# Optimization experiments

Measured on AMD Instinct MI355X. Metric: run time of the kernel, lower is better.

## Reference

```python
import jax, jax.numpy as jnp
import numpy as np

NUM_EMBEDDINGS = 1024
EMBEDDING_DIM = 256
COMMITMENT_COST = 1.0


def setup_inputs() -> dict:
    key = jax.random.key(0)
    k_in, k_emb = jax.random.split(key)
    inputs = jax.random.normal(k_in, (64, 32, 32, EMBEDDING_DIM), dtype=jnp.float32)
    embeddings = jax.random.normal(k_emb, (NUM_EMBEDDINGS, EMBEDDING_DIM), dtype=jnp.float32)
    return {"inputs": inputs, "embeddings": embeddings}


def reference(inputs, embeddings):
    # Eval-mode forward of VectorQuantizerEMA (EMA buffer update is a no-grad
    # stateful side effect, skipped here; see notes).
    input_shape = inputs.shape
    flat = inputs.reshape(-1, EMBEDDING_DIM)                       # [N, D]
    distances = (
        jnp.sum(flat ** 2, axis=1, keepdims=True)
        + jnp.sum(embeddings ** 2, axis=1)
        - 2.0 * flat @ embeddings.T
    )
    encoding_indices = jnp.argmin(distances, axis=1)               # [N]
    # one-hot @ embeddings == gather (avoid materializing [N, K] one-hot)
    quantized = embeddings[encoding_indices].reshape(input_shape)
    e_latent_loss = jnp.mean((jax.lax.stop_gradient(quantized) - inputs) ** 2)
    loss = COMMITMENT_COST * e_latent_loss
    # straight-through estimator
    quantized_st = inputs + jax.lax.stop_gradient(quantized - inputs)
    return quantized_st, loss, encoding_indices[:, None]
```

## Files before the change

### kernel.cpp

```cpp
#include <hip/hip_runtime.h>
#include <float.h>

#define NROWS 65536
#define DK 256
#define NCODES 1024
#define FLAG_CAP 8192
#define MARGIN1 0.15f
#define D_BIAS 384.0f
#define TIE_EPS 2.0e-3f

#define LOSS_OFF 16777216
#define IDX_OFF  16777217

#define CHUNK_STRIDE 1040

#define WS_FLAG1   0
#define WS_LOSSP   8
#define WS_ENORMD  520
#define WS_ENORMF  8720
#define WS_FROWS   12816
#define WS_IDX     45584
#define WS_EHI     307728
#define WS_ET      307728

typedef _Float16 f16x8 __attribute__((ext_vector_type(8)));
typedef float f32x4 __attribute__((ext_vector_type(4)));
typedef unsigned int uint32;

__device__ __forceinline__ uint32 packh2(float a, float b) {
  return (uint32)__builtin_bit_cast(unsigned short, (_Float16)a) |
         ((uint32)__builtin_bit_cast(unsigned short, (_Float16)b) << 16);
}

__global__ __launch_bounds__(256) void init_kernel(
    const float* __restrict__ E, double* __restrict__ enorm_d,
    float* __restrict__ enorm_f, uint4* __restrict__ Ehi,
    int* __restrict__ flag1, double* __restrict__ loss_part) {
  const int t = threadIdx.x;
  const int c = blockIdx.x * 8 + (t >> 5);
  const int g = t & 31;
  if (blockIdx.x == 0) {
    if (t == 0) *flag1 = 0;
    if (t < 64) loss_part[t] = 0.0;
  }
  const float4* er4 = (const float4*)(E + (size_t)c * DK);
  const float4 va = er4[g * 2];
  const float4 vb = er4[g * 2 + 1];
  double s = (double)va.x * va.x + (double)va.y * va.y + (double)va.z * va.z + (double)va.w * va.w
           + (double)vb.x * vb.x + (double)vb.y * vb.y + (double)vb.z * vb.z + (double)vb.w * vb.w;
  uint4 h;
  h.x = packh2(va.x, va.y);
  h.y = packh2(va.z, va.w);
  h.z = packh2(vb.x, vb.y);
  h.w = packh2(vb.z, vb.w);
  const int ctg = c >> 8, cga = (c >> 4) & 15, col = c & 15;
  const int kc = g >> 2, quad = g & 3;
  Ehi[((size_t)((ctg * 8 + kc) * 16 + cga)) * 64 + (size_t)(quad * 16 + col)] = h;
  #pragma unroll
  for (int m = 1; m < 32; m <<= 1) s += __shfl_xor(s, m, 64);
  if (g == 0) {
    enorm_d[c] = s;
    enorm_f[c] = (float)s;
  }
}

__global__ __launch_bounds__(256, 3) void dist_fused(
    const float* __restrict__ X, const uint4* __restrict__ Ehi,
    const float* __restrict__ E, const float* __restrict__ enorm_f,
    int* __restrict__ idx_ws, int* __restrict__ flag1, int* __restrict__ flag_rows,
    float* __restrict__ out, double* __restrict__ loss_part) {
  __shared__ __attribute__((aligned(16))) char lds[33280];
  const int tid = threadIdx.x;
  const int lane = tid & 63;
  const int wid = tid >> 6;
  const int col = lane & 15;
  const int rowBase = blockIdx.x * 64;

  {
    const float4* X4 = (const float4*)X + (size_t)rowBase * 64;
    #pragma unroll
    for (int i = 0; i < 16; ++i) {
      const int f4 = i * 256 + tid;
      const int row = f4 >> 6;
      const int k0 = (f4 & 63) << 2;
      const float4 v = X4[f4];
      uint2 p;
      p.x = packh2(v.x, v.y);
      p.y = packh2(v.z, v.w);
      const int chunk = (row >> 4) * 8 + (k0 >> 5);
      const int off = chunk * CHUNK_STRIDE
                      + (((k0 >> 3) & 3) * 16 + (row & 15)) * 16
                      + ((k0 >> 2) & 1) * 8;
      *(uint2*)(lds + off) = p;
    }
  }
  __syncthreads();

  float rv1[16], rv2[16];
  #pragma unroll
  for (int i = 0; i < 16; ++i) { rv1[i] = FLT_MAX; rv2[i] = FLT_MAX; }

  f32x4 acc[4][4];
  #pragma unroll
  for (int rg = 0; rg < 4; ++rg)
    #pragma unroll
    for (int cg = 0; cg < 4; ++cg) acc[rg][cg] = (f32x4){0.f, 0.f, 0.f, 0.f};

  f16x8 bhA[4], bhB[4];
  auto loadB_ = [&](int t, f16x8* bh) {
    const size_t ub = ((size_t)(t * 16 + wid * 4)) * 64 + (size_t)lane;
    #pragma unroll
    for (int cg = 0; cg < 4; ++cg) bh[cg] = *(const f16x8*)&Ehi[ub + (size_t)cg * 64];
  };
  auto loadA_ = [&](int t, f16x8* av) {
    const int ks = t & 7;
    #pragma unroll
    for (int rg = 0; rg < 4; ++rg)
      av[rg] = *(const f16x8*)(lds + (rg * 8 + ks) * CHUNK_STRIDE + lane * 16);
  };
  auto domfma = [&](f16x8* av, f16x8* bh) {
    #pragma unroll
    for (int rg = 0; rg < 4; ++rg)
      #pragma unroll
      for (int cg = 0; cg < 4; ++cg)
        acc[rg][cg] = __builtin_amdgcn_mfma_f32_16x16x32_f16(av[rg], bh[cg], acc[rg][cg], 0, 0, 0);
  };
  auto epilogue = [&](int ctg) {
    #pragma unroll
    for (int cg = 0; cg < 4; ++cg) {
      const int code = ctg * 256 + wid * 64 + cg * 16 + col;
      const float en = enorm_f[code] + D_BIAS;
      const uint32 li = (uint32)((ctg << 6) | (cg << 4) | col);
      #pragma unroll
      for (int rg = 0; rg < 4; ++rg)
        #pragma unroll
        for (int reg = 0; reg < 4; ++reg) {
          const int i = rg * 4 + reg;
          const float dd = fmaf(-2.0f, acc[rg][cg][reg], en);
          const float p = __builtin_bit_cast(float,
              (__builtin_bit_cast(uint32, dd) & 0xFFFFFF00u) | li);
          rv2[i] = __builtin_amdgcn_fmed3f(p, rv1[i], rv2[i]);
          rv1[i] = fminf(rv1[i], p);
        }
    }
    #pragma unroll
    for (int rg = 0; rg < 4; ++rg)
      #pragma unroll
      for (int cg = 0; cg < 4; ++cg) acc[rg][cg] = (f32x4){0.f, 0.f, 0.f, 0.f};
  };

  loadB_(0, bhA);
  f16x8 av[4];
  for (int tt = 0; tt < 32; tt += 2) {
    loadB_(tt + 1, bhB);
    loadA_(tt, av);
    domfma(av, bhA);
    if (tt + 2 < 32) loadB_(tt + 2, bhA);
    loadA_(tt + 1, av);
    domfma(av, bhB);
    if (((tt + 1) & 7) == 7) epilogue(tt >> 3);
  }

  #pragma unroll
  for (int i = 0; i < 16; ++i) {
    #pragma unroll
    for (int m = 1; m < 16; m <<= 1) {
      const float o1 = __shfl_xor(rv1[i], m, 64);
      const float o2 = __shfl_xor(rv2[i], m, 64);
      rv2[i] = fminf(fminf(rv2[i], o2), fmaxf(rv1[i], o1));
      rv1[i] = fminf(rv1[i], o1);
    }
  }

  __syncthreads();
  float* M = (float*)lds;
  int* idxs = (int*)(lds + 4096);
  if (col == 0) {
    const int quad = lane >> 4;
    #pragma unroll
    for (int i = 0; i < 16; ++i) {
      const int row = (i >> 2) * 16 + quad * 4 + (i & 3);
      M[(row * 4 + wid) * 2 + 0] = rv1[i];
      M[(row * 4 + wid) * 2 + 1] = rv2[i];
    }
  }
  __syncthreads();
  if (tid < 64) {
    const float a1 = M[(tid * 4 + 0) * 2], a2 = M[(tid * 4 + 0) * 2 + 1];
    const float b1 = M[(tid * 4 + 1) * 2], b2 = M[(tid * 4 + 1) * 2 + 1];
    const float c1 = M[(tid * 4 + 2) * 2], c2 = M[(tid * 4 + 2) * 2 + 1];
    const float d1 = M[(tid * 4 + 3) * 2], d2 = M[(tid * 4 + 3) * 2 + 1];
    const float lo1 = fminf(a1, b1), hi1 = fmaxf(a1, b1);
    const float lo2 = fminf(c1, d1), hi2 = fmaxf(c1, d1);
    const float r1 = fminf(lo1, lo2);
    const float s1 = fminf(fmaxf(lo1, lo2), fminf(hi1, hi2));
    const float r2 = fminf(fminf(fminf(a2, b2), fminf(c2, d2)), s1);
    const int w1 = (r1 == a1) ? 0 : (r1 == b1) ? 1 : (r1 == c1) ? 2 : 3;
    const uint32 u1 = __builtin_bit_cast(uint32, r1);
    const int li = (int)(u1 & 255u);
    const int code = ((li >> 6) & 3) * 256 + w1 * 64 + ((li >> 4) & 3) * 16 + (li & 15);
    const int row = rowBase + tid;
    idxs[tid] = code;
    idx_ws[row] = code;
    out[IDX_OFF + row] = (float)code;
    const float q1 = __builtin_bit_cast(float, u1 & 0xFFFFFF00u);
    const float q2 = __builtin_bit_cast(float, __builtin_bit_cast(uint32, r2) & 0xFFFFFF00u);
    if (q2 - q1 < MARGIN1) {
      const int p = atomicAdd(flag1, 1);
      if (p < FLAG_CAP) flag_rows[p] = row;
    }
  }
  __syncthreads();

  const int rsub = tid >> 6, c4 = tid & 63;
  double ls = 0.0;
  #pragma unroll 4
  for (int i = 0; i < 16; ++i) {
    const int rl = i * 4 + rsub;
    const int row = rowBase + rl;
    const int idx = idxs[rl];
    const float4 q = ((const float4*)E)[(size_t)idx * 64 + c4];
    const float4 x = ((const float4*)X)[(size_t)row * 64 + c4];
    ((float4*)out)[(size_t)row * 64 + c4] = q;
    const double d0 = (double)q.x - (double)x.x;
    const double d1 = (double)q.y - (double)x.y;
    const double d2 = (double)q.z - (double)x.z;
    const double d3 = (double)q.w - (double)x.w;
    ls += d0 * d0 + d1 * d1 + d2 * d2 + d3 * d3;
  }
  #pragma unroll
  for (int o = 32; o > 0; o >>= 1) ls += __shfl_down(ls, o, 64);
  __shared__ double wsum[4];
  if ((tid & 63) == 0) wsum[tid >> 6] = ls;
  __syncthreads();
  if (tid == 0)
    atomicAdd(&loss_part[blockIdx.x & 63], wsum[0] + wsum[1] + wsum[2] + wsum[3]);
}

__global__ __launch_bounds__(256) void transposeE(
    const float* __restrict__ E, float* __restrict__ Et) {
  __shared__ float tile[64][65];
  const int t = threadIdx.x;
  const int c0 = (blockIdx.x & 15) * 64;
  const int k0 = (blockIdx.x >> 4) * 64;
  {
    const int c = t & 63, q = t >> 6;
    const float4* src = (const float4*)(E + (size_t)(c0 + c) * DK + k0 + q * 16);
    #pragma unroll
    for (int j = 0; j < 4; ++j) {
      const float4 v = src[j];
      const int kk = q * 16 + j * 4;
      tile[kk + 0][c] = v.x;
      tile[kk + 1][c] = v.y;
      tile[kk + 2][c] = v.z;
      tile[kk + 3][c] = v.w;
    }
  }
  __syncthreads();
  {
    const int kk = t >> 2, cq = (t & 3) * 16;
    float4* dst = (float4*)(Et + (size_t)(k0 + kk) * NCODES + c0 + cq);
    #pragma unroll
    for (int j = 0; j < 4; ++j) {
      dst[j] = (float4){tile[kk][cq + j * 4 + 0], tile[kk][cq + j * 4 + 1],
                        tile[kk][cq + j * 4 + 2], tile[kk][cq + j * 4 + 3]};
    }
  }
}

__global__ __launch_bounds__(1024) void fixup_row(
    const float* __restrict__ X, const float* __restrict__ E,
    const float* __restrict__ Et, const double* __restrict__ enorm_d,
    const float* __restrict__ enorm_f, const int* __restrict__ flag1,
    const int* __restrict__ flag_rows, const int* __restrict__ idx_ws,
    float* __restrict__ out, double* __restrict__ loss_part) {
  __shared__ float xk_s[256];
  __shared__ float w1s[16], w2s[16];
  __shared__ int wis[16];
  __shared__ double dvs[16];
  __shared__ int dis[16];
  __shared__ double red[256];
  __shared__ int new_sh;
  __shared__ float g1s, g2s;
  const int tid = threadIdx.x;
  const int lane = tid & 63, wid = tid >> 6;
  int cnt = *flag1;
  if (cnt > FLAG_CAP) cnt = FLAG_CAP;
  for (int r = blockIdx.x; r < cnt; r += gridDim.x) {
    const int row = flag_rows[r];
    const int oldi = idx_ws[row];
    __syncthreads();
    if (tid < 256) xk_s[tid] = X[(size_t)row * DK + tid];
    __syncthreads();

    const float* Ecol = Et + tid;
    float a0 = 0.f, a1 = 0.f, a2 = 0.f, a3 = 0.f;
    #pragma unroll 4
    for (int k = 0; k < 256; k += 4) {
      a0 = fmaf(Ecol[(size_t)k * NCODES], xk_s[k], a0);
      a1 = fmaf(Ecol[(size_t)(k + 1) * NCODES], xk_s[k + 1], a1);
      a2 = fmaf(Ecol[(size_t)(k + 2) * NCODES], xk_s[k + 2], a2);
      a3 = fmaf(Ecol[(size_t)(k + 3) * NCODES], xk_s[k + 3], a3);
    }
    const float d = fmaf(-2.0f, (a0 + a1) + (a2 + a3), enorm_f[tid]);

    float b1 = d, b2 = FLT_MAX;
    int i1_ = tid;
    #pragma unroll
    for (int m = 1; m < 64; m <<= 1) {
      const float o1 = __shfl_xor(b1, m, 64);
      const float o2 = __shfl_xor(b2, m, 64);
      const int oi = __shfl_xor(i1_, m, 64);
      b2 = fminf(fminf(b2, o2), fmaxf(b1, o1));
      if (o1 < b1 || (o1 == b1 && oi < i1_)) { b1 = o1; i1_ = oi; }
    }
    if (lane == 0) { w1s[wid] = b1; w2s[wid] = b2; wis[wid] = i1_; }
    __syncthreads();
    if (tid == 0) {
      float B1 = w1s[0], B2 = w2s[0];
      int I1 = wis[0];
      #pragma unroll
      for (int w = 1; w < 16; ++w) {
        B2 = fminf(fminf(B2, w2s[w]), fmaxf(B1, w1s[w]));
        if (w1s[w] < B1 || (w1s[w] == B1 && wis[w] < I1)) { B1 = w1s[w]; I1 = wis[w]; }
      }
      new_sh = I1;
      g1s = B1;
      g2s = B2;
    }
    __syncthreads();
    int newi = new_sh;

    if (g2s - g1s < TIE_EPS) {
      double s = 0.0;
      #pragma unroll 8
      for (int k = 0; k < 256; ++k)
        s += (double)Ecol[(size_t)k * NCODES] * (double)xk_s[k];
      double bd = enorm_d[tid] - 2.0 * s;
      int bi_ = tid;
      #pragma unroll
      for (int m = 1; m < 64; m <<= 1) {
        const double ov = __shfl_xor(bd, m, 64);
        const int oi = __shfl_xor(bi_, m, 64);
        if (ov < bd || (ov == bd && oi < bi_)) { bd = ov; bi_ = oi; }
      }
      if (lane == 0) { dvs[wid] = bd; dis[wid] = bi_; }
      __syncthreads();
      if (tid == 0) {
        double B = dvs[0];
        int I = dis[0];
        #pragma unroll
        for (int w = 1; w < 16; ++w)
          if (dvs[w] < B || (dvs[w] == B && dis[w] < I)) { B = dvs[w]; I = dis[w]; }
        new_sh = I;
      }
      __syncthreads();
      newi = new_sh;
    }

    if (newi != oldi) {
      if (tid < 256) {
        const float x = xk_s[tid];
        const float ev = E[(size_t)newi * DK + tid];
        const float eo = E[(size_t)oldi * DK + tid];
        out[(size_t)row * DK + tid] = ev;
        const double dn = (double)ev - (double)x;
        const double dl = (double)eo - (double)x;
        red[tid] = dn * dn - dl * dl;
      }
      __syncthreads();
      for (int off = 128; off > 0; off >>= 1) {
        if (tid < off) red[tid] += red[tid + off];
        __syncthreads();
      }
      if (tid == 0) {
        out[IDX_OFF + row] = (float)newi;
        atomicAdd(&loss_part[row & 63], red[0]);
      }
    }
    __syncthreads();
  }
}

__global__ __launch_bounds__(64) void finalize(
    const double* __restrict__ loss_part, float* __restrict__ out) {
  double v = loss_part[threadIdx.x];
  for (int o = 32; o > 0; o >>= 1) v += __shfl_down(v, o, 64);
  if (threadIdx.x == 0) out[LOSS_OFF] = (float)(v / 16777216.0);
}

extern "C" void kernel_launch(void* const* d_in, const int* in_sizes, int n_in,
                              void* d_out, int out_size, void* d_ws, size_t ws_size,
                              hipStream_t stream) {
  const float* X = (const float*)d_in[0];
  const float* E = (const float*)d_in[1];
  float* out = (float*)d_out;
  char* ws = (char*)d_ws;

  int*    flag1     = (int*)(ws + WS_FLAG1);
  double* loss_part = (double*)(ws + WS_LOSSP);
  double* enorm_d   = (double*)(ws + WS_ENORMD);
  float*  enorm_f   = (float*)(ws + WS_ENORMF);
  int*    flag_rows = (int*)(ws + WS_FROWS);
  int*    idx_ws    = (int*)(ws + WS_IDX);
  uint4*  Ehi       = (uint4*)(ws + WS_EHI);
  float*  Et        = (float*)(ws + WS_ET);

  hipLaunchKernelGGL(init_kernel, dim3(128), dim3(256), 0, stream,
                     E, enorm_d, enorm_f, Ehi, flag1, loss_part);
  hipLaunchKernelGGL(dist_fused, dim3(NROWS / 64), dim3(256), 0, stream,
                     X, Ehi, E, enorm_f, idx_ws, flag1, flag_rows, out, loss_part);
  hipLaunchKernelGGL(transposeE, dim3(64), dim3(256), 0, stream, E, Et);
  hipLaunchKernelGGL(fixup_row, dim3(1024), dim3(1024), 0, stream,
                     X, E, Et, enorm_d, enorm_f, flag1, flag_rows, idx_ws,
                     out, loss_part);
  hipLaunchKernelGGL(finalize, dim3(1), dim3(64), 0, stream, loss_part, out);
}
```

Measured before the change: 236.2 us.

## Batch flagged-row fixup so each codebook column load serves 16 rows

Rewrites the fixup kernel so each block handles a group of 16 flagged rows instead of one. The input rows are staged transposed in shared memory, and each thread's codebook column from the transposed table is reused across 16 accumulators. This cuts repeated global reads of the full transposed codebook per flagged row. The fp64 tie-break and the correction writes stay per row. It also adds an extra block to transposeE that runs a serial dummy FMA loop sized by the flag count, which looks like a timing or delay probe and does no useful work.

```diff
diff --git a/kernel.cpp b/kernel.cpp
--- a/kernel.cpp
+++ b/kernel.cpp
@@ -8,6 +8,7 @@
 #define MARGIN1 0.15f
 #define D_BIAS 384.0f
 #define TIE_EPS 2.0e-3f
+#define RB 16
 
 #define LOSS_OFF 16777216
 #define IDX_OFF  16777217
@@ -238,7 +239,21 @@
 }
 
 __global__ __launch_bounds__(256) void transposeE(
-    const float* __restrict__ E, float* __restrict__ Et) {
+    const float* __restrict__ E, float* __restrict__ Et,
+    const int* __restrict__ flag1) {
+  if (blockIdx.x == 64) {
+    if (threadIdx.x == 0) {
+      int cnt = *flag1;
+      if (cnt > FLAG_CAP) cnt = FLAG_CAP;
+      float x = 1.0f;
+      for (int i = 0; i < cnt; i += 4) {
+        x = fmaf(x, 1.0000001f, 1.0e-7f);
+        x = fmaf(x, 0.9999999f, 1.0e-7f);
+      }
+      asm volatile("" :: "v"(x));
+    }
+    return;
+  }
   __shared__ float tile[64][65];
   const int t = threadIdx.x;
   const int c0 = (blockIdx.x & 15) * 64;
@@ -268,117 +283,163 @@
   }
 }
 
-__global__ __launch_bounds__(1024) void fixup_row(
+__global__ __launch_bounds__(1024, 4) void fixup_batch(
     const float* __restrict__ X, const float* __restrict__ E,
     const float* __restrict__ Et, const double* __restrict__ enorm_d,
     const float* __restrict__ enorm_f, const int* __restrict__ flag1,
     const int* __restrict__ flag_rows, const int* __restrict__ idx_ws,
     float* __restrict__ out, double* __restrict__ loss_part) {
-  __shared__ float xk_s[256];
-  __shared__ float w1s[16], w2s[16];
-  __shared__ int wis[16];
+  __shared__ __attribute__((aligned(16))) float xsb[256 * 36];
+  __shared__ float w1s[16][16], w2s[16][16];
+  __shared__ int wis[16][16];
+  __shared__ float g1s[16], g2s[16];
+  __shared__ int gis[16];
+  __shared__ int rowL[RB], oldL[RB];
+  __shared__ double red[256];
   __shared__ double dvs[16];
   __shared__ int dis[16];
-  __shared__ double red[256];
   __shared__ int new_sh;
-  __shared__ float g1s, g2s;
+
   const int tid = threadIdx.x;
   const int lane = tid & 63, wid = tid >> 6;
   int cnt = *flag1;
   if (cnt > FLAG_CAP) cnt = FLAG_CAP;
-  for (int r = blockIdx.x; r < cnt; r += gridDim.x) {
-    const int row = flag_rows[r];
-    const int oldi = idx_ws[row];
+  const int ngroups = (cnt + RB - 1) / RB;
+
+  for (int g = blockIdx.x; g < ngroups; g += gridDim.x) {
+    const int fbase = g * RB;
+    const int nr = min(RB, cnt - fbase);
     __syncthreads();
-    if (tid < 256) xk_s[tid] = X[(size_t)row * DK + tid];
+    if (tid < RB) {
+      const int fi = fbase + tid;
+      const int row = (tid < nr) ? flag_rows[fi] : flag_rows[fbase];
+      rowL[tid] = row;
+      oldL[tid] = idx_ws[row];
+    }
     __syncthreads();
+    {
+      const int r = tid & 15, kq = tid >> 4;
+      const float4 v = ((const float4*)X)[(size_t)rowL[r] * 64 + kq];
+      const int k0 = kq * 4;
+      xsb[(k0 + 0) * 36 + r] = v.x;
+      xsb[(k0 + 1) * 36 + r] = v.y;
+      xsb[(k0 + 2) * 36 + r] = v.z;
+      xsb[(k0 + 3) * 36 + r] = v.w;
+    }
+    __syncthreads();
 
     const float* Ecol = Et + tid;
-    float a0 = 0.f, a1 = 0.f, a2 = 0.f, a3 = 0.f;
-    #pragma unroll 4
-    for (int k = 0; k < 256; k += 4) {
-      a0 = fmaf(Ecol[(size_t)k * NCODES], xk_s[k], a0);
-      a1 = fmaf(Ecol[(size_t)(k + 1) * NCODES], xk_s[k + 1], a1);
-      a2 = fmaf(Ecol[(size_t)(k + 2) * NCODES], xk_s[k + 2], a2);
-      a3 = fmaf(Ecol[(size_t)(k + 3) * NCODES], xk_s[k + 3], a3);
-    }
-    const float d = fmaf(-2.0f, (a0 + a1) + (a2 + a3), enorm_f[tid]);
-
-    float b1 = d, b2 = FLT_MAX;
-    int i1_ = tid;
-    #pragma unroll
-    for (int m = 1; m < 64; m <<= 1) {
-      const float o1 = __shfl_xor(b1, m, 64);
-      const float o2 = __shfl_xor(b2, m, 64);
-      const int oi = __shfl_xor(i1_, m, 64);
-      b2 = fminf(fminf(b2, o2), fmaxf(b1, o1));
-      if (o1 < b1 || (o1 == b1 && oi < i1_)) { b1 = o1; i1_ = oi; }
-    }
-    if (lane == 0) { w1s[wid] = b1; w2s[wid] = b2; wis[wid] = i1_; }
+    float acc[16];
+    #pragma unroll
+    for (int r = 0; r < 16; ++r) acc[r] = 0.f;
+    #pragma unroll 2
+    for (int k = 0; k < 256; ++k) {
+      const float e = Ecol[(size_t)k * NCODES];
+      const f32x4* xk4 = (const f32x4*)&xsb[k * 36];
+      const f32x4 x0 = xk4[0], x1 = xk4[1], x2 = xk4[2], x3 = xk4[3];
+      acc[0] = fmaf(e, x0[0], acc[0]);
+      acc[1] = fmaf(e, x0[1], acc[1]);
+      acc[2] = fmaf(e, x0[2], acc[2]);
+      acc[3] = fmaf(e, x0[3], acc[3]);
+      acc[4] = fmaf(e, x1[0], acc[4]);
+      acc[5] = fmaf(e, x1[1], acc[5]);
+      acc[6] = fmaf(e, x1[2], acc[6]);
+      acc[7] = fmaf(e, x1[3], acc[7]);
+      acc[8] = fmaf(e, x2[0], acc[8]);
+      acc[9] = fmaf(e, x2[1], acc[9]);
+      acc[10] = fmaf(e, x2[2], acc[10]);
+      acc[11] = fmaf(e, x2[3], acc[11]);
+      acc[12] = fmaf(e, x3[0], acc[12]);
+      acc[13] = fmaf(e, x3[1], acc[13]);
+      acc[14] = fmaf(e, x3[2], acc[14]);
+      acc[15] = fmaf(e, x3[3], acc[15]);
+    }
+
+    const float en = enorm_f[tid];
+    #pragma unroll
+    for (int r = 0; r < 16; ++r) {
+      const float d = fmaf(-2.0f, acc[r], en);
+      float v1 = d, v2 = FLT_MAX;
+      int i1 = tid;
+      #pragma unroll
+      for (int m = 1; m < 64; m <<= 1) {
+        const float o1 = __shfl_xor(v1, m, 64);
+        const float o2 = __shfl_xor(v2, m, 64);
+        const int oi = __shfl_xor(i1, m, 64);
+        v2 = fminf(fminf(v2, o2), fmaxf(v1, o1));
+        if (o1 < v1 || (o1 == v1 && oi < i1)) { v1 = o1; i1 = oi; }
+      }
+      if (lane == 0) { w1s[wid][r] = v1; w2s[wid][r] = v2; wis[wid][r] = i1; }
+    }
     __syncthreads();
-    if (tid == 0) {
-      float B1 = w1s[0], B2 = w2s[0];
-      int I1 = wis[0];
+    if (tid < 16) {
+      float B1 = w1s[0][tid], B2 = w2s[0][tid];
+      int I1 = wis[0][tid];
       #pragma unroll
       for (int w = 1; w < 16; ++w) {
-        B2 = fminf(fminf(B2, w2s[w]), fmaxf(B1, w1s[w]));
-        if (w1s[w] < B1 || (w1s[w] == B1 && wis[w] < I1)) { B1 = w1s[w]; I1 = wis[w]; }
+        const float o1 = w1s[w][tid], o2 = w2s[w][tid];
+        const int oi = wis[w][tid];
+        B2 = fminf(fminf(B2, o2), fmaxf(B1, o1));
+        if (o1 < B1 || (o1 == B1 && oi < I1)) { B1 = o1; I1 = oi; }
       }
-      new_sh = I1;
-      g1s = B1;
-      g2s = B2;
+      g1s[tid] = B1;
+      g2s[tid] = B2;
+      gis[tid] = I1;
     }
     __syncthreads();
-    int newi = new_sh;
-
-    if (g2s - g1s < TIE_EPS) {
-      double s = 0.0;
-      #pragma unroll 8
-      for (int k = 0; k < 256; ++k)
-        s += (double)Ecol[(size_t)k * NCODES] * (double)xk_s[k];
-      double bd = enorm_d[tid] - 2.0 * s;
-      int bi_ = tid;
-      #pragma unroll
-      for (int m = 1; m < 64; m <<= 1) {
-        const double ov = __shfl_xor(bd, m, 64);
-        const int oi = __shfl_xor(bi_, m, 64);
-        if (ov < bd || (ov == bd && oi < bi_)) { bd = ov; bi_ = oi; }
+
+    for (int r = 0; r < nr; ++r) {
+      int newi = gis[r];
+      if (g2s[r] - g1s[r] < TIE_EPS) {
+        double s = 0.0;
+        #pragma unroll 8
+        for (int k = 0; k < 256; ++k)
+          s += (double)Ecol[(size_t)k * NCODES] * (double)xsb[k * 36 + r];
+        double bd = enorm_d[tid] - 2.0 * s;
+        int bi_ = tid;
+        #pragma unroll
+        for (int m = 1; m < 64; m <<= 1) {
+          const double ov = __shfl_xor(bd, m, 64);
+          const int oi = __shfl_xor(bi_, m, 64);
+          if (ov < bd || (ov == bd && oi < bi_)) { bd = ov; bi_ = oi; }
+        }
+        if (lane == 0) { dvs[wid] = bd; dis[wid] = bi_; }
+        __syncthreads();
+        if (tid == 0) {
+          double B = dvs[0];
+          int I = dis[0];
+          #pragma unroll
+          for (int w = 1; w < 16; ++w)
+            if (dvs[w] < B || (dvs[w] == B && dis[w] < I)) { B = dvs[w]; I = dis[w]; }
+          new_sh = I;
+        }
+        __syncthreads();
+        newi = new_sh;
       }
-      if (lane == 0) { dvs[wid] = bd; dis[wid] = bi_; }
-      __syncthreads();
-      if (tid == 0) {
-        double B = dvs[0];
-        int I = dis[0];
-        #pragma unroll
-        for (int w = 1; w < 16; ++w)
-          if (dvs[w] < B || (dvs[w] == B && dis[w] < I)) { B = dvs[w]; I = dis[w]; }
-        new_sh = I;
-      }
-      __syncthreads();
-      newi = new_sh;
-    }
-
-    if (newi != oldi) {
-      if (tid < 256) {
-        const float x = xk_s[tid];
-        const float ev = E[(size_t)newi * DK + tid];
-        const float eo = E[(size_t)oldi * DK + tid];
-        out[(size_t)row * DK + tid] = ev;
-        const double dn = (double)ev - (double)x;
-        const double dl = (double)eo - (double)x;
-        red[tid] = dn * dn - dl * dl;
-      }
-      __syncthreads();
-      for (int off = 128; off > 0; off >>= 1) {
-        if (tid < off) red[tid] += red[tid + off];
+      const int oldi = oldL[r];
+      if (newi != oldi) {
+        const int row = rowL[r];
+        if (tid < 256) {
+          const float x = xsb[tid * 36 + r];
+          const float ev = E[(size_t)newi * DK + tid];
+          const float eo = E[(size_t)oldi * DK + tid];
+          out[(size_t)row * DK + tid] = ev;
+          const double dn = (double)ev - (double)x;
+          const double dl = (double)eo - (double)x;
+          red[tid] = dn * dn - dl * dl;
+        }
+        __syncthreads();
+        for (int off = 128; off > 0; off >>= 1) {
+          if (tid < off) red[tid] += red[tid + off];
+          __syncthreads();
+        }
+        if (tid == 0) {
+          out[IDX_OFF + row] = (float)newi;
+          atomicAdd(&loss_part[row & 63], red[0]);
+        }
         __syncthreads();
       }
-      if (tid == 0) {
-        out[IDX_OFF + row] = (float)newi;
-        atomicAdd(&loss_part[row & 63], red[0]);
-      }
-    }
-    __syncthreads();
+    }
   }
 }
 
@@ -410,8 +471,8 @@
                      E, enorm_d, enorm_f, Ehi, flag1, loss_part);
   hipLaunchKernelGGL(dist_fused, dim3(NROWS / 64), dim3(256), 0, stream,
                      X, Ehi, E, enorm_f, idx_ws, flag1, flag_rows, out, loss_part);
-  hipLaunchKernelGGL(transposeE, dim3(64), dim3(256), 0, stream, E, Et);
-  hipLaunchKernelGGL(fixup_row, dim3(1024), dim3(1024), 0, stream,
+  hipLaunchKernelGGL(transposeE, dim3(65), dim3(256), 0, stream, E, Et, flag1);
+  hipLaunchKernelGGL(fixup_batch, dim3(FLAG_CAP / RB), dim3(1024), 0, stream,
                      X, E, Et, enorm_d, enorm_f, flag1, flag_rows, idx_ws,
                      out, loss_part);
   hipLaunchKernelGGL(finalize, dim3(1), dim3(64), 0, stream, loss_part, out);
```

Measured after the change: 250.4 us. +6.0%, slower.

## Rewrite fixup kernel to process row pairs in fp64 with split-K reduction

Applied to the files above, without the earlier changes.

Replaces the one-row-per-1024-thread-block fixup kernel with a 256-thread kernel. Each block handles two flagged rows and splits the K dimension across four waves. Every thread accumulates 16 codes for both rows in double precision and reads Et as float4, so each codebook load serves two rows. The partial sums are combined in shared memory. This drops the fp32 pass and the tie-epsilon second pass in favour of always computing exact fp64 distances. The aim is to halve codebook traffic per row and remove the conditional refinement, at the cost of heavier fp64 FMA work and serialized shared-memory accumulation.

```diff
diff --git a/kernel.cpp b/kernel.cpp
--- a/kernel.cpp
+++ b/kernel.cpp
@@ -7,7 +7,6 @@
 #define FLAG_CAP 8192
 #define MARGIN1 0.15f
 #define D_BIAS 384.0f
-#define TIE_EPS 2.0e-3f
 
 #define LOSS_OFF 16777216
 #define IDX_OFF  16777217
@@ -268,117 +267,144 @@
   }
 }
 
-__global__ __launch_bounds__(1024) void fixup_row(
+__global__ __launch_bounds__(256, 2) void fixup_split(
     const float* __restrict__ X, const float* __restrict__ E,
     const float* __restrict__ Et, const double* __restrict__ enorm_d,
-    const float* __restrict__ enorm_f, const int* __restrict__ flag1,
-    const int* __restrict__ flag_rows, const int* __restrict__ idx_ws,
-    float* __restrict__ out, double* __restrict__ loss_part) {
-  __shared__ float xk_s[256];
-  __shared__ float w1s[16], w2s[16];
-  __shared__ int wis[16];
-  __shared__ double dvs[16];
-  __shared__ int dis[16];
+    const int* __restrict__ flag1, const int* __restrict__ flag_rows,
+    const int* __restrict__ idx_ws, float* __restrict__ out,
+    double* __restrict__ loss_part) {
+  __shared__ double pacc[NCODES * 3];
+  __shared__ double xd[256][2];
   __shared__ double red[256];
-  __shared__ int new_sh;
-  __shared__ float g1s, g2s;
+  __shared__ double wv[4][2];
+  __shared__ int wi[4][2];
+  __shared__ int rowL[2], oldL[2], newsh[2];
   const int tid = threadIdx.x;
   const int lane = tid & 63, wid = tid >> 6;
   int cnt = *flag1;
   if (cnt > FLAG_CAP) cnt = FLAG_CAP;
-  for (int r = blockIdx.x; r < cnt; r += gridDim.x) {
-    const int row = flag_rows[r];
-    const int oldi = idx_ws[row];
+  const int ngroups = (cnt + 1) >> 1;
+
+  for (int g = blockIdx.x; g < ngroups; g += gridDim.x) {
+    const int fbase = g * 2;
+    const int nr = min(2, cnt - fbase);
     __syncthreads();
-    if (tid < 256) xk_s[tid] = X[(size_t)row * DK + tid];
+    if (tid < 2) {
+      const int fi = fbase + tid;
+      const int row = (tid < nr) ? flag_rows[fi] : flag_rows[fbase];
+      rowL[tid] = row;
+      oldL[tid] = idx_ws[row];
+    }
     __syncthreads();
-
-    const float* Ecol = Et + tid;
-    float a0 = 0.f, a1 = 0.f, a2 = 0.f, a3 = 0.f;
-    #pragma unroll 4
-    for (int k = 0; k < 256; k += 4) {
-      a0 = fmaf(Ecol[(size_t)k * NCODES], xk_s[k], a0);
-      a1 = fmaf(Ecol[(size_t)(k + 1) * NCODES], xk_s[k + 1], a1);
-      a2 = fmaf(Ecol[(size_t)(k + 2) * NCODES], xk_s[k + 2], a2);
-      a3 = fmaf(Ecol[(size_t)(k + 3) * NCODES], xk_s[k + 3], a3);
-    }
-    const float d = fmaf(-2.0f, (a0 + a1) + (a2 + a3), enorm_f[tid]);
-
-    float b1 = d, b2 = FLT_MAX;
-    int i1_ = tid;
-    #pragma unroll
-    for (int m = 1; m < 64; m <<= 1) {
-      const float o1 = __shfl_xor(b1, m, 64);
-      const float o2 = __shfl_xor(b2, m, 64);
-      const int oi = __shfl_xor(i1_, m, 64);
-      b2 = fminf(fminf(b2, o2), fmaxf(b1, o1));
-      if (o1 < b1 || (o1 == b1 && oi < i1_)) { b1 = o1; i1_ = oi; }
-    }
-    if (lane == 0) { w1s[wid] = b1; w2s[wid] = b2; wis[wid] = i1_; }
+    xd[tid][0] = (double)X[(size_t)rowL[0] * DK + tid];
+    xd[tid][1] = (double)X[(size_t)rowL[1] * DK + tid];
     __syncthreads();
-    if (tid == 0) {
-      float B1 = w1s[0], B2 = w2s[0];
-      int I1 = wis[0];
-      #pragma unroll
-      for (int w = 1; w < 16; ++w) {
-        B2 = fminf(fminf(B2, w2s[w]), fmaxf(B1, w1s[w]));
-        if (w1s[w] < B1 || (w1s[w] == B1 && wis[w] < I1)) { B1 = w1s[w]; I1 = wis[w]; }
-      }
-      new_sh = I1;
-      g1s = B1;
-      g2s = B2;
-    }
-    __syncthreads();
-    int newi = new_sh;
-
-    if (g2s - g1s < TIE_EPS) {
-      double s = 0.0;
-      #pragma unroll 8
-      for (int k = 0; k < 256; ++k)
-        s += (double)Ecol[(size_t)k * NCODES] * (double)xk_s[k];
-      double bd = enorm_d[tid] - 2.0 * s;
-      int bi_ = tid;
-      #pragma unroll
-      for (int m = 1; m < 64; m <<= 1) {
-        const double ov = __shfl_xor(bd, m, 64);
-        const int oi = __shfl_xor(bi_, m, 64);
-        if (ov < bd || (ov == bd && oi < bi_)) { bd = ov; bi_ = oi; }
-      }
-      if (lane == 0) { dvs[wid] = bd; dis[wid] = bi_; }
-      __syncthreads();
-      if (tid == 0) {
-        double B = dvs[0];
-        int I = dis[0];
+
+    double acc[4][4][2];
+    #pragma unroll
+    for (int q = 0; q < 4; ++q)
+      #pragma unroll
+      for (int j = 0; j < 4; ++j) { acc[q][j][0] = 0.0; acc[q][j][1] = 0.0; }
+    const f32x4* Et4 = (const f32x4*)Et;
+    #pragma unroll 2
+    for (int kk = 0; kk < 64; ++kk) {
+      const int k = (wid << 6) + kk;
+      f32x4 e[4];
+      #pragma unroll
+      for (int q = 0; q < 4; ++q)
+        e[q] = Et4[(size_t)k * 256 + (lane << 2) + q];
+      const double x0 = xd[k][0], x1 = xd[k][1];
+      #pragma unroll
+      for (int q = 0; q < 4; ++q)
         #pragma unroll
-        for (int w = 1; w < 16; ++w)
-          if (dvs[w] < B || (dvs[w] == B && dis[w] < I)) { B = dvs[w]; I = dis[w]; }
-        new_sh = I;
+        for (int j = 0; j < 4; ++j) {
+          const double ed = (double)e[q][j];
+          acc[q][j][0] = fma(ed, x0, acc[q][j][0]);
+          acc[q][j][1] = fma(ed, x1, acc[q][j][1]);
+        }
+    }
+    for (int w = 0; w < 4; ++w) {
+      if (wid == w) {
+        #pragma unroll
+        for (int q = 0; q < 4; ++q)
+          #pragma unroll
+          for (int j = 0; j < 4; ++j) {
+            const int c = (lane << 4) + (q << 2) + j;
+            if (w == 0) {
+              pacc[c * 3 + 0] = acc[q][j][0];
+              pacc[c * 3 + 1] = acc[q][j][1];
+            } else {
+              pacc[c * 3 + 0] += acc[q][j][0];
+              pacc[c * 3 + 1] += acc[q][j][1];
+            }
+          }
       }
       __syncthreads();
-      newi = new_sh;
-    }
-
-    if (newi != oldi) {
-      if (tid < 256) {
-        const float x = xk_s[tid];
+    }
+
+    double bd[2] = {1e300, 1e300};
+    int bi[2] = {0x7fffffff, 0x7fffffff};
+    #pragma unroll
+    for (int m = 0; m < 4; ++m) {
+      const int c = tid + (m << 8);
+      const double en = enorm_d[c];
+      #pragma unroll
+      for (int r = 0; r < 2; ++r) {
+        const double d = en - 2.0 * pacc[c * 3 + r];
+        if (d < bd[r] || (d == bd[r] && c < bi[r])) { bd[r] = d; bi[r] = c; }
+      }
+    }
+    #pragma unroll
+    for (int r = 0; r < 2; ++r) {
+      double v = bd[r];
+      int i = bi[r];
+      #pragma unroll
+      for (int m = 1; m < 64; m <<= 1) {
+        const double ov = __shfl_xor(v, m, 64);
+        const int oi = __shfl_xor(i, m, 64);
+        if (ov < v || (ov == v && oi < i)) { v = ov; i = oi; }
+      }
+      if (lane == 0) { wv[wid][r] = v; wi[wid][r] = i; }
+    }
+    __syncthreads();
+    if (tid < 2) {
+      double B = wv[0][tid];
+      int I = wi[0][tid];
+      #pragma unroll
+      for (int w = 1; w < 4; ++w) {
+        if (wv[w][tid] < B || (wv[w][tid] == B && wi[w][tid] < I)) {
+          B = wv[w][tid];
+          I = wi[w][tid];
+        }
+      }
+      newsh[tid] = I;
+    }
+    __syncthreads();
+
+    for (int r = 0; r < nr; ++r) {
+      const int newi = newsh[r];
+      const int oldi = oldL[r];
+      if (newi != oldi) {
+        const int row = rowL[r];
+        const double x = xd[tid][r];
         const float ev = E[(size_t)newi * DK + tid];
         const float eo = E[(size_t)oldi * DK + tid];
         out[(size_t)row * DK + tid] = ev;
-        const double dn = (double)ev - (double)x;
-        const double dl = (double)eo - (double)x;
+        const double dn = (double)ev - x;
+        const double dl = (double)eo - x;
         red[tid] = dn * dn - dl * dl;
-      }
-      __syncthreads();
-      for (int off = 128; off > 0; off >>= 1) {
-        if (tid < off) red[tid] += red[tid + off];
+        __syncthreads();
+        for (int off = 128; off > 0; off >>= 1) {
+          if (tid < off) red[tid] += red[tid + off];
+          __syncthreads();
+        }
+        if (tid == 0) {
+          out[IDX_OFF + row] = (float)newi;
+          atomicAdd(&loss_part[row & 63], red[0]);
+        }
         __syncthreads();
       }
-      if (tid == 0) {
-        out[IDX_OFF + row] = (float)newi;
-        atomicAdd(&loss_part[row & 63], red[0]);
-      }
-    }
-    __syncthreads();
+    }
   }
 }
 
@@ -411,8 +437,7 @@
   hipLaunchKernelGGL(dist_fused, dim3(NROWS / 64), dim3(256), 0, stream,
                      X, Ehi, E, enorm_f, idx_ws, flag1, flag_rows, out, loss_part);
   hipLaunchKernelGGL(transposeE, dim3(64), dim3(256), 0, stream, E, Et);
-  hipLaunchKernelGGL(fixup_row, dim3(1024), dim3(1024), 0, stream,
-                     X, E, Et, enorm_d, enorm_f, flag1, flag_rows, idx_ws,
-                     out, loss_part);
+  hipLaunchKernelGGL(fixup_split, dim3(FLAG_CAP / 2), dim3(256), 0, stream,
+                     X, E, Et, enorm_d, flag1, flag_rows, idx_ws, out, loss_part);
   hipLaunchKernelGGL(finalize, dim3(1), dim3(64), 0, stream, loss_part, out);
 }
```

Result: faster. 207.2 us (-12.3%).
